# Optimization experiments

Measured on AMD Instinct MI355X. Metric: run time of the kernel, lower is better.

The kernel has to match this reference:

```python
import jax, jax.numpy as jnp
import numpy as np

EMBED_DIM = 1024
NUM_HEADS = 16
HEAD_DIM = EMBED_DIM // NUM_HEADS
SCALE = float(np.sqrt(HEAD_DIM))


def setup_inputs() -> dict:
    key = jax.random.key(0)
    ks = jax.random.split(key, 7)
    B, S, E = 2, 2048, EMBED_DIM
    query = jax.random.normal(ks[0], (B, S, E), dtype=jnp.float32)
    key_t = jax.random.normal(ks[1], (B, S, E), dtype=jnp.float32)
    value = jax.random.normal(ks[2], (B, S, E), dtype=jnp.float32)
    # nn.Linear(E, E, bias=False): weight shape (out, in); y = x @ W.T
    std = 1.0 / np.sqrt(E)
    Wq = jax.random.uniform(ks[3], (E, E), jnp.float32, -std, std)
    Wk = jax.random.uniform(ks[4], (E, E), jnp.float32, -std, std)
    Wv = jax.random.uniform(ks[5], (E, E), jnp.float32, -std, std)
    Wo = jax.random.uniform(ks[6], (E, E), jnp.float32, -std, std)
    return {"query": query, "key": key_t, "value": value,
            "Wq": Wq, "Wk": Wk, "Wv": Wv, "Wo": Wo}


def reference(query, key, value, Wq, Wk, Wv, Wo):
    B, S, E = query.shape
    H, D = NUM_HEADS, HEAD_DIM
    q = (query @ Wq.T).reshape(B, S, H, D).transpose(0, 2, 1, 3)  # [B,H,S,D]
    k = (key @ Wk.T).reshape(B, S, H, D).transpose(0, 2, 1, 3)
    v = (value @ Wv.T).reshape(B, S, H, D).transpose(0, 2, 1, 3)
    scores = jnp.einsum('bhqd,bhkd->bhqk', q, k) / SCALE  # [B,H,S,S]
    attn = jax.nn.softmax(scores, axis=-1)
    out = jnp.einsum('bhqk,bhkd->bhqd', attn, v)  # [B,H,S,D]
    out = out.transpose(0, 2, 1, 3).reshape(B, S, E)
    return out @ Wo.T
```

## Files before the change

### kernel.cpp

```cpp
#include <hip/hip_runtime.h>
#include <hip/hip_bf16.h>
#include <math.h>

typedef float f32x4 __attribute__((ext_vector_type(4)));
typedef __bf16 bf16x8 __attribute__((ext_vector_type(8)));
typedef unsigned short u16;
typedef u16 u16x8 __attribute__((ext_vector_type(8)));
typedef u16 u16x4 __attribute__((ext_vector_type(4)));

__device__ __forceinline__ u16 f2bf(float f) {
    unsigned u = __builtin_bit_cast(unsigned, f);
    u = (u + 0x7fffu + ((u >> 16) & 1u)) >> 16;
    return (u16)u;
}
__device__ __forceinline__ unsigned pack2_rhu(float a, float b) {
    return __builtin_amdgcn_perm(__builtin_bit_cast(unsigned, b) + 0x8000u,
                                 __builtin_bit_cast(unsigned, a) + 0x8000u,
                                 0x07060302u);
}

#if __has_builtin(__builtin_amdgcn_exp2f)
#define EXP2(x) __builtin_amdgcn_exp2f(x)
#else
#define EXP2(x) exp2f(x)
#endif

__device__ __forceinline__ void gload16(const u16* g, u16* l) {
    __builtin_amdgcn_global_load_lds(
        (const __attribute__((address_space(1))) unsigned int*)(g),
        (__attribute__((address_space(3))) unsigned int*)(l), 16, 0, 0);
}

__global__ __launch_bounds__(256) void cast_all(
    const float* __restrict__ q, const float* __restrict__ k, const float* __restrict__ v,
    const float* __restrict__ wq, const float* __restrict__ wk, const float* __restrict__ wv,
    const float* __restrict__ wo, u16* __restrict__ dst) {
    int i = blockIdx.x * 256 + threadIdx.x;
    const float* src;
    int off;
    if (i < 3145728) {
        int seg = i >> 20;
        src = (seg == 0) ? q : (seg == 1) ? k : v;
        off = i - (seg << 20);
    } else {
        int j = (i - 3145728) >> 18;
        src = (j == 0) ? wq : (j == 1) ? wk : (j == 2) ? wv : wo;
        off = (i - 3145728) - (j << 18);
    }
    float4 val = ((const float4*)src)[off];
    u16x4 o4;
    o4.x = f2bf(val.x); o4.y = f2bf(val.y); o4.z = f2bf(val.z); o4.w = f2bf(val.w);
    ((u16x4*)dst)[i] = o4;
}

__global__ __launch_bounds__(256) void qkv_gemm(
    const u16* __restrict__ Xq, const u16* __restrict__ Xk, const u16* __restrict__ Xv,
    const u16* __restrict__ Wq, const u16* __restrict__ Wk, const u16* __restrict__ Wv,
    u16* __restrict__ Qo, u16* __restrict__ Ko, u16* __restrict__ Vto) {
    constexpr int K = 1024;
    constexpr int BUF = 128 * 64;
    const int blk = blockIdx.x;
    const int xb = blk / 96;
    const int zb = (blk % 96) >> 5;
    const int yb = blk & 31;
    const int z = zb;
    const u16* __restrict__ A = (z == 0) ? Xq : (z == 1) ? Xk : Xv;
    const u16* __restrict__ W = (z == 0) ? Wq : (z == 1) ? Wk : Wv;
    u16* __restrict__ Out = (z == 0) ? Qo : (z == 1) ? Ko : Vto;

    __shared__ __align__(16) u16 As[2 * BUF];
    __shared__ __align__(16) u16 Bs[2 * BUF];

    const int t = threadIdx.x;
    const int lane = t & 63, wave = t >> 6;
    const int quad = lane >> 4, c = lane & 15, cx = c & 7;
    const int wr = (wave >> 1) * 64, wc = (wave & 1) * 64;
    const int rowA0 = yb * 128;
    const int colB0 = xb * 128;

    const int l3 = lane >> 3, l7 = lane & 7;
    const int chs = (l7 ^ l3) << 3;
    const u16* gA[4];
    const u16* gB[4];
    u16* lA[4];
    u16* lB[4];
#pragma unroll
    for (int i = 0; i < 4; ++i) {
        int row = wave * 32 + i * 8 + l3;
        gA[i] = A + (size_t)(rowA0 + row) * K + chs;
        gB[i] = W + (size_t)(colB0 + row) * K + chs;
        lA[i] = As + (wave * 256 + i * 64) * 8;
        lB[i] = Bs + (wave * 256 + i * 64) * 8;
    }

    const f32x4 zero4 = {0.f, 0.f, 0.f, 0.f};
    f32x4 acc[4][4];
#pragma unroll
    for (int i = 0; i < 4; ++i)
#pragma unroll
        for (int j = 0; j < 4; ++j) acc[i][j] = zero4;

#pragma unroll
    for (int i = 0; i < 4; ++i) {
        gload16(gA[i], lA[i]);
        gload16(gB[i], lB[i]);
    }

    for (int it = 0; it < 16; ++it) {
        __syncthreads();
        if (it + 1 < 16) {
            const int nb = ((it + 1) & 1) * BUF;
            const int kt = (it + 1) * 64;
#pragma unroll
            for (int i = 0; i < 4; ++i) {
                gload16(gA[i] + kt, lA[i] + nb);
                gload16(gB[i] + kt, lB[i] + nb);
            }
        }
        const int so = (it & 1) * BUF;
#pragma unroll
        for (int ks = 0; ks < 2; ++ks) {
            const int co = ((ks * 4 + quad) ^ cx) << 3;
            bf16x8 af[4], bfr[4];
#pragma unroll
            for (int i = 0; i < 4; ++i)
                af[i] = *(const bf16x8*)(As + so + (wr + i * 16 + c) * 64 + co);
#pragma unroll
            for (int j = 0; j < 4; ++j)
                bfr[j] = *(const bf16x8*)(Bs + so + (wc + j * 16 + c) * 64 + co);
            if (z == 2) {
#pragma unroll
                for (int i = 0; i < 4; ++i)
#pragma unroll
                    for (int j = 0; j < 4; ++j)
                        acc[i][j] = __builtin_amdgcn_mfma_f32_16x16x32_bf16(bfr[j], af[i], acc[i][j], 0, 0, 0);
            } else {
#pragma unroll
                for (int i = 0; i < 4; ++i)
#pragma unroll
                    for (int j = 0; j < 4; ++j)
                        acc[i][j] = __builtin_amdgcn_mfma_f32_16x16x32_bf16(af[i], bfr[j], acc[i][j], 0, 0, 0);
            }
        }
    }

    const float scale = (z == 0) ? 0.18033688011112042f : 1.0f;
#pragma unroll
    for (int i = 0; i < 4; ++i) {
#pragma unroll
        for (int j = 0; j < 4; ++j) {
#pragma unroll
            for (int r = 0; r < 4; ++r) {
                float v = acc[i][j][r];
                if (z == 2) {
                    int n = colB0 + wc + j * 16 + quad * 4 + r;
                    int m = rowA0 + wr + i * 16 + c;
                    int b = m >> 11, s = m & 2047, h = n >> 6, d = n & 63;
                    Out[((((b << 4) | h) << 6) + d) * 2048 + s] = f2bf(v);
                } else {
                    int m = rowA0 + wr + i * 16 + quad * 4 + r;
                    int n = colB0 + wc + j * 16 + c;
                    int b = m >> 11, s = m & 2047, h = n >> 6, d = n & 63;
                    Out[((((b << 4) | h) * 2048 + s) << 6) + d] = f2bf(v * scale);
                }
            }
        }
    }
}

__global__ __launch_bounds__(256) void out_gemm(const u16* __restrict__ A,
                                                const u16* __restrict__ W,
                                                float* __restrict__ Out) {
    constexpr int K = 1024;
    constexpr int ABUF = 64 * 64;
    constexpr int BBUF = 128 * 64;
    __shared__ __align__(16) u16 As[2 * ABUF];
    __shared__ __align__(16) u16 Bs[2 * BBUF];
    const int blk = blockIdx.x;
    const int yb = blk & 63;
    const int xb = blk >> 6;
    const int t = threadIdx.x;
    const int lane = t & 63, wave = t >> 6;
    const int quad = lane >> 4, c = lane & 15, cx = c & 7;
    const int wr = (wave >> 1) * 32, wc = (wave & 1) * 64;
    const int rowA0 = yb * 64;
    const int colB0 = xb * 128;

    const int l3 = lane >> 3, l7 = lane & 7;
    const int chs = (l7 ^ l3) << 3;
    const u16* gA[2];
    const u16* gB[4];
    u16* lA[2];
    u16* lB[4];
#pragma unroll
    for (int i = 0; i < 2; ++i) {
        int row = wave * 16 + i * 8 + l3;
        gA[i] = A + (size_t)(rowA0 + row) * K + chs;
        lA[i] = As + (wave * 128 + i * 64) * 8;
    }
#pragma unroll
    for (int i = 0; i < 4; ++i) {
        int row = wave * 32 + i * 8 + l3;
        gB[i] = W + (size_t)(colB0 + row) * K + chs;
        lB[i] = Bs + (wave * 256 + i * 64) * 8;
    }

    const f32x4 zero4 = {0.f, 0.f, 0.f, 0.f};
    f32x4 acc[2][4];
#pragma unroll
    for (int i = 0; i < 2; ++i)
#pragma unroll
        for (int j = 0; j < 4; ++j) acc[i][j] = zero4;

#pragma unroll
    for (int i = 0; i < 2; ++i) gload16(gA[i], lA[i]);
#pragma unroll
    for (int i = 0; i < 4; ++i) gload16(gB[i], lB[i]);

    for (int it = 0; it < 16; ++it) {
        __syncthreads();
        if (it + 1 < 16) {
            const int kt = (it + 1) * 64;
            const int nsel = (it + 1) & 1;
#pragma unroll
            for (int i = 0; i < 2; ++i) gload16(gA[i] + kt, lA[i] + nsel * ABUF);
#pragma unroll
            for (int i = 0; i < 4; ++i) gload16(gB[i] + kt, lB[i] + nsel * BBUF);
        }
        const int soA = (it & 1) * ABUF;
        const int soB = (it & 1) * BBUF;
#pragma unroll
        for (int ks = 0; ks < 2; ++ks) {
            const int co = ((ks * 4 + quad) ^ cx) << 3;
            bf16x8 af[2], bfr[4];
#pragma unroll
            for (int i = 0; i < 2; ++i)
                af[i] = *(const bf16x8*)(As + soA + (wr + i * 16 + c) * 64 + co);
#pragma unroll
            for (int j = 0; j < 4; ++j)
                bfr[j] = *(const bf16x8*)(Bs + soB + (wc + j * 16 + c) * 64 + co);
#pragma unroll
            for (int i = 0; i < 2; ++i)
#pragma unroll
                for (int j = 0; j < 4; ++j)
                    acc[i][j] = __builtin_amdgcn_mfma_f32_16x16x32_bf16(af[i], bfr[j], acc[i][j], 0, 0, 0);
        }
    }
#pragma unroll
    for (int i = 0; i < 2; ++i)
#pragma unroll
        for (int j = 0; j < 4; ++j)
#pragma unroll
            for (int r = 0; r < 4; ++r) {
                int m = rowA0 + wr + i * 16 + quad * 4 + r;
                int n = colB0 + wc + j * 16 + c;
                Out[(m << 10) + n] = acc[i][j][r];
            }
}

__global__ __launch_bounds__(512) void flash_attn(const u16* __restrict__ Qp,
                                                  const u16* __restrict__ Kp,
                                                  const u16* __restrict__ Vt,
                                                  u16* __restrict__ Ob) {
    constexpr int S = 2048;
    const int blk = blockIdx.x;
    const int bh = ((blk & 7) << 2) | ((blk >> 3) & 3);
    const int b = bh >> 4, h = bh & 15;
    const int t = threadIdx.x, wave = t >> 6, lane = t & 63;
    const int quad = lane >> 4, c = lane & 15, cx = c & 7;
    const int qw = (blk >> 5) * 256 + wave * 32;
    const u16* Qb = Qp + (bh * S + qw) * 64;
    const u16* Kb = Kp + (bh * S) * 64;
    const u16* Vb = Vt + bh * 64 * S;

    __shared__ __align__(16) u16 Ks[2][64 * 64];
    __shared__ __align__(16) u16 Vs[2][64 * 64];
    __shared__ __align__(16) u16 Ps[8][32 * 64];
    u16* Pw = &Ps[wave][0];

    bf16x8 qf[2][2];
#pragma unroll
    for (int qt = 0; qt < 2; ++qt)
#pragma unroll
        for (int hf = 0; hf < 2; ++hf)
            qf[qt][hf] = *(const bf16x8*)(Qb + (qt * 16 + c) * 64 + hf * 32 + quad * 8);

    u16x8 ou;
#pragma unroll
    for (int i = 0; i < 8; ++i) ou[i] = 0x3F80;
    const bf16x8 onesf = __builtin_bit_cast(bf16x8, ou);

    const int l3 = lane >> 3, l7 = lane & 7;
    const int chs = (l7 ^ l3) << 3;
    const int row = wave * 8 + l3;
    const u16* gK = Kb + row * 64 + chs;
    const u16* gV = Vb + row * 2048 + chs;
    const int lbase = wave * 512;

    gload16(gK, &Ks[0][lbase]);
    gload16(gV, &Vs[0][lbase]);
    __syncthreads();

    const f32x4 zero4 = {0.f, 0.f, 0.f, 0.f};
    f32x4 o[2][4];
    f32x4 ol[2];
#pragma unroll
    for (int qt = 0; qt < 2; ++qt) {
        ol[qt] = zero4;
#pragma unroll
        for (int t2 = 0; t2 < 4; ++t2) o[qt][t2] = zero4;
    }

    const int co0 = (quad ^ cx) << 3, co1 = ((4 + quad) ^ cx) << 3;

    for (int it = 0; it < S / 64; ++it) {
        const int cur = it & 1;
        if (it + 1 < S / 64) {
            gload16(gK + (it + 1) * 4096, &Ks[cur ^ 1][lbase]);
            gload16(gV + (it + 1) * 64, &Vs[cur ^ 1][lbase]);
        }
        const u16* Kc = &Ks[cur][0];
        const u16* Vc = &Vs[cur][0];
        f32x4 sc[4][2];
#pragma unroll
        for (int kt = 0; kt < 4; ++kt) {
            const int krow = (kt * 16 + c) * 64;
            bf16x8 kf0 = *(const bf16x8*)(Kc + krow + co0);
            bf16x8 kf1 = *(const bf16x8*)(Kc + krow + co1);
#pragma unroll
            for (int qt = 0; qt < 2; ++qt) {
                f32x4 zz = zero4;
                zz = __builtin_amdgcn_mfma_f32_16x16x32_bf16(kf0, qf[qt][0], zz, 0, 0, 0);
                zz = __builtin_amdgcn_mfma_f32_16x16x32_bf16(kf1, qf[qt][1], zz, 0, 0, 0);
                sc[kt][qt] = zz;
            }
        }
#pragma unroll
        for (int kt = 0; kt < 4; ++kt) {
            const int pchunk = ((kt * 2 + (quad >> 1)) ^ cx) << 3;
#pragma unroll
            for (int qt = 0; qt < 2; ++qt) {
                float p0 = EXP2(sc[kt][qt][0]);
                float p1 = EXP2(sc[kt][qt][1]);
                float p2 = EXP2(sc[kt][qt][2]);
                float p3 = EXP2(sc[kt][qt][3]);
                uint2 pk;
                pk.x = pack2_rhu(p0, p1);
                pk.y = pack2_rhu(p2, p3);
                *(uint2*)(Pw + (qt * 16 + c) * 64 + pchunk + (quad & 1) * 4) = pk;
            }
        }
        __asm__ __volatile__("s_waitcnt lgkmcnt(0)" ::: "memory");
        bf16x8 pf[2][2];
#pragma unroll
        for (int qt = 0; qt < 2; ++qt) {
            pf[qt][0] = *(const bf16x8*)(Pw + (qt * 16 + c) * 64 + co0);
            pf[qt][1] = *(const bf16x8*)(Pw + (qt * 16 + c) * 64 + co1);
        }
#pragma unroll
        for (int qt = 0; qt < 2; ++qt) {
            ol[qt] = __builtin_amdgcn_mfma_f32_16x16x32_bf16(pf[qt][0], onesf, ol[qt], 0, 0, 0);
            ol[qt] = __builtin_amdgcn_mfma_f32_16x16x32_bf16(pf[qt][1], onesf, ol[qt], 0, 0, 0);
        }
#pragma unroll
        for (int t2 = 0; t2 < 4; ++t2) {
            const int vrow = (t2 * 16 + c) * 64;
            bf16x8 vf0 = *(const bf16x8*)(Vc + vrow + co0);
            bf16x8 vf1 = *(const bf16x8*)(Vc + vrow + co1);
#pragma unroll
            for (int qt = 0; qt < 2; ++qt) {
                o[qt][t2] = __builtin_amdgcn_mfma_f32_16x16x32_bf16(pf[qt][0], vf0, o[qt][t2], 0, 0, 0);
                o[qt][t2] = __builtin_amdgcn_mfma_f32_16x16x32_bf16(pf[qt][1], vf1, o[qt][t2], 0, 0, 0);
            }
        }
        __syncthreads();
    }
#pragma unroll
    for (int qt = 0; qt < 2; ++qt)
#pragma unroll
        for (int r = 0; r < 4; ++r) {
            float inv = 1.f / ol[qt][r];
            int rw = qw + qt * 16 + quad * 4 + r;
            int base = ((b * S + rw) * 16 + h) * 64;
#pragma unroll
            for (int t2 = 0; t2 < 4; ++t2)
                Ob[base + t2 * 16 + c] = f2bf(o[qt][t2][r] * inv);
        }
}

extern "C" void kernel_launch(void* const* d_in, const int* in_sizes, int n_in,
                              void* d_out, int out_size, void* d_ws, size_t ws_size,
                              hipStream_t stream) {
    const float* q  = (const float*)d_in[0];
    const float* k  = (const float*)d_in[1];
    const float* v  = (const float*)d_in[2];
    const float* wq = (const float*)d_in[3];
    const float* wk = (const float*)d_in[4];
    const float* wv = (const float*)d_in[5];
    const float* wo = (const float*)d_in[6];

    u16* ws = (u16*)d_ws;
    u16* qb  = ws;
    u16* kb  = ws + 4194304;
    u16* vb  = ws + 8388608;
    u16* wqb = ws + 12582912;
    u16* wkb = ws + 13631488;
    u16* wvb = ws + 14680064;
    u16* wob = ws + 15728640;
    u16* Qp  = ws + 16777216;
    u16* Kp  = ws + 20971520;
    u16* Vtp = ws + 25165824;
    u16* Obf = ws + 29360128;

    cast_all<<<16384, 256, 0, stream>>>(q, k, v, wq, wk, wv, wo, ws);

    qkv_gemm<<<768, 256, 0, stream>>>(qb, kb, vb, wqb, wkb, wvb, Qp, Kp, Vtp);

    flash_attn<<<256, 512, 0, stream>>>(Qp, Kp, Vtp, Obf);

    out_gemm<<<512, 256, 0, stream>>>(Obf, wob, (float*)d_out);
}
```

Baseline: 216.5 us.

## Keep P in registers using 16x16x16 MFMA and halve attention block size

The attention kernel no longer writes the exp'd score tile P to LDS and reads it back. The score MFMA output layout is reused directly as the A operand of 16x16x16 bf16 MFMAs, and V fragments are read with matching swizzled 4-element loads. Blocks shrink from 8 waves to 4 with twice as many blocks, and each thread issues two K/V async loads per tile. This removes the P LDS round trip and its waitcnt, but doubles the MFMA instruction count at half the K depth and adds more, smaller LDS reads for V.

```diff
diff --git a/kernel.cpp b/kernel.cpp
--- a/kernel.cpp
+++ b/kernel.cpp
@@ -4,6 +4,8 @@
 
 typedef float f32x4 __attribute__((ext_vector_type(4)));
 typedef __bf16 bf16x8 __attribute__((ext_vector_type(8)));
+typedef __bf16 bf16x4 __attribute__((ext_vector_type(4)));
+typedef short s16x4 __attribute__((ext_vector_type(4)));
 typedef unsigned short u16;
 typedef u16 u16x8 __attribute__((ext_vector_type(8)));
 typedef u16 u16x4 __attribute__((ext_vector_type(4)));
@@ -24,6 +26,15 @@
 #else
 #define EXP2(x) exp2f(x)
 #endif
+
+__device__ __forceinline__ f32x4 mfma16(bf16x4 a, bf16x4 b, f32x4 c) {
+#if __has_builtin(__builtin_amdgcn_mfma_f32_16x16x16_bf16)
+    return __builtin_amdgcn_mfma_f32_16x16x16_bf16(a, b, c, 0, 0, 0);
+#else
+    return __builtin_amdgcn_mfma_f32_16x16x16bf16_1k(
+        __builtin_bit_cast(s16x4, a), __builtin_bit_cast(s16x4, b), c, 0, 0, 0);
+#endif
+}
 
 __device__ __forceinline__ void gload16(const u16* g, u16* l) {
     __builtin_amdgcn_global_load_lds(
@@ -258,25 +269,24 @@
             }
 }
 
-__global__ __launch_bounds__(512) void flash_attn(const u16* __restrict__ Qp,
+__global__ __launch_bounds__(256) void flash_attn(const u16* __restrict__ Qp,
                                                   const u16* __restrict__ Kp,
                                                   const u16* __restrict__ Vt,
                                                   u16* __restrict__ Ob) {
     constexpr int S = 2048;
     const int blk = blockIdx.x;
-    const int bh = ((blk & 7) << 2) | ((blk >> 3) & 3);
+    const int j = blk & 31;
+    const int bh = ((j & 7) << 2) | (j >> 3);
     const int b = bh >> 4, h = bh & 15;
     const int t = threadIdx.x, wave = t >> 6, lane = t & 63;
     const int quad = lane >> 4, c = lane & 15, cx = c & 7;
-    const int qw = (blk >> 5) * 256 + wave * 32;
+    const int qw = (blk >> 5) * 128 + wave * 32;
     const u16* Qb = Qp + (bh * S + qw) * 64;
     const u16* Kb = Kp + (bh * S) * 64;
     const u16* Vb = Vt + bh * 64 * S;
 
     __shared__ __align__(16) u16 Ks[2][64 * 64];
     __shared__ __align__(16) u16 Vs[2][64 * 64];
-    __shared__ __align__(16) u16 Ps[8][32 * 64];
-    u16* Pw = &Ps[wave][0];
 
     bf16x8 qf[2][2];
 #pragma unroll
@@ -285,20 +295,28 @@
         for (int hf = 0; hf < 2; ++hf)
             qf[qt][hf] = *(const bf16x8*)(Qb + (qt * 16 + c) * 64 + hf * 32 + quad * 8);
 
-    u16x8 ou;
-#pragma unroll
-    for (int i = 0; i < 8; ++i) ou[i] = 0x3F80;
-    const bf16x8 onesf = __builtin_bit_cast(bf16x8, ou);
+    u16x4 ou;
+#pragma unroll
+    for (int i = 0; i < 4; ++i) ou[i] = 0x3F80;
+    const bf16x4 ones4 = __builtin_bit_cast(bf16x4, ou);
 
     const int l3 = lane >> 3, l7 = lane & 7;
     const int chs = (l7 ^ l3) << 3;
-    const int row = wave * 8 + l3;
-    const u16* gK = Kb + row * 64 + chs;
-    const u16* gV = Vb + row * 2048 + chs;
-    const int lbase = wave * 512;
-
-    gload16(gK, &Ks[0][lbase]);
-    gload16(gV, &Vs[0][lbase]);
+    const u16* gK[2];
+    const u16* gV[2];
+    int lbase[2];
+#pragma unroll
+    for (int i = 0; i < 2; ++i) {
+        int row = wave * 16 + i * 8 + l3;
+        gK[i] = Kb + row * 64 + chs;
+        gV[i] = Vb + row * 2048 + chs;
+        lbase[i] = (wave * 128 + i * 64) * 8;
+    }
+#pragma unroll
+    for (int i = 0; i < 2; ++i) {
+        gload16(gK[i], &Ks[0][lbase[i]]);
+        gload16(gV[i], &Vs[0][lbase[i]]);
+    }
     __syncthreads();
 
     const f32x4 zero4 = {0.f, 0.f, 0.f, 0.f};
@@ -316,8 +334,11 @@
     for (int it = 0; it < S / 64; ++it) {
         const int cur = it & 1;
         if (it + 1 < S / 64) {
-            gload16(gK + (it + 1) * 4096, &Ks[cur ^ 1][lbase]);
-            gload16(gV + (it + 1) * 64, &Vs[cur ^ 1][lbase]);
+#pragma unroll
+            for (int i = 0; i < 2; ++i) {
+                gload16(gK[i] + (it + 1) * 4096, &Ks[cur ^ 1][lbase[i]]);
+                gload16(gV[i] + (it + 1) * 64, &Vs[cur ^ 1][lbase[i]]);
+            }
         }
         const u16* Kc = &Ks[cur][0];
         const u16* Vc = &Vs[cur][0];
@@ -335,9 +356,9 @@
                 sc[kt][qt] = zz;
             }
         }
-#pragma unroll
-        for (int kt = 0; kt < 4; ++kt) {
-            const int pchunk = ((kt * 2 + (quad >> 1)) ^ cx) << 3;
+        bf16x4 pa[4][2];
+#pragma unroll
+        for (int kt = 0; kt < 4; ++kt)
 #pragma unroll
             for (int qt = 0; qt < 2; ++qt) {
                 float p0 = EXP2(sc[kt][qt][0]);
@@ -347,30 +368,23 @@
                 uint2 pk;
                 pk.x = pack2_rhu(p0, p1);
                 pk.y = pack2_rhu(p2, p3);
-                *(uint2*)(Pw + (qt * 16 + c) * 64 + pchunk + (quad & 1) * 4) = pk;
-            }
-        }
-        __asm__ __volatile__("s_waitcnt lgkmcnt(0)" ::: "memory");
-        bf16x8 pf[2][2];
-#pragma unroll
-        for (int qt = 0; qt < 2; ++qt) {
-            pf[qt][0] = *(const bf16x8*)(Pw + (qt * 16 + c) * 64 + co0);
-            pf[qt][1] = *(const bf16x8*)(Pw + (qt * 16 + c) * 64 + co1);
-        }
-#pragma unroll
-        for (int qt = 0; qt < 2; ++qt) {
-            ol[qt] = __builtin_amdgcn_mfma_f32_16x16x32_bf16(pf[qt][0], onesf, ol[qt], 0, 0, 0);
-            ol[qt] = __builtin_amdgcn_mfma_f32_16x16x32_bf16(pf[qt][1], onesf, ol[qt], 0, 0, 0);
-        }
+                pa[kt][qt] = __builtin_bit_cast(bf16x4, pk);
+            }
+#pragma unroll
+        for (int kt = 0; kt < 4; ++kt)
+#pragma unroll
+            for (int qt = 0; qt < 2; ++qt)
+                ol[qt] = mfma16(pa[kt][qt], ones4, ol[qt]);
 #pragma unroll
         for (int t2 = 0; t2 < 4; ++t2) {
             const int vrow = (t2 * 16 + c) * 64;
-            bf16x8 vf0 = *(const bf16x8*)(Vc + vrow + co0);
-            bf16x8 vf1 = *(const bf16x8*)(Vc + vrow + co1);
-#pragma unroll
-            for (int qt = 0; qt < 2; ++qt) {
-                o[qt][t2] = __builtin_amdgcn_mfma_f32_16x16x32_bf16(pf[qt][0], vf0, o[qt][t2], 0, 0, 0);
-                o[qt][t2] = __builtin_amdgcn_mfma_f32_16x16x32_bf16(pf[qt][1], vf1, o[qt][t2], 0, 0, 0);
+#pragma unroll
+            for (int kt = 0; kt < 4; ++kt) {
+                const int vphys = ((kt * 2 + (quad >> 1)) ^ cx) << 3;
+                bf16x4 vf = *(const bf16x4*)(Vc + vrow + vphys + (quad & 1) * 4);
+#pragma unroll
+                for (int qt = 0; qt < 2; ++qt)
+                    o[qt][t2] = mfma16(pa[kt][qt], vf, o[qt][t2]);
             }
         }
         __syncthreads();
@@ -380,8 +394,8 @@
 #pragma unroll
         for (int r = 0; r < 4; ++r) {
             float inv = 1.f / ol[qt][r];
-            int rw = qw + qt * 16 + quad * 4 + r;
-            int base = ((b * S + rw) * 16 + h) * 64;
+            int row = qw + qt * 16 + quad * 4 + r;
+            int base = ((b * S + row) * 16 + h) * 64;
 #pragma unroll
             for (int t2 = 0; t2 < 4; ++t2)
                 Ob[base + t2 * 16 + c] = f2bf(o[qt][t2][r] * inv);
@@ -416,7 +430,7 @@
 
     qkv_gemm<<<768, 256, 0, stream>>>(qb, kb, vb, wqb, wkb, wvb, Qp, Kp, Vtp);
 
-    flash_attn<<<256, 512, 0, stream>>>(Qp, Kp, Vtp, Obf);
+    flash_attn<<<512, 256, 0, stream>>>(Qp, Kp, Vtp, Obf);
 
     out_gemm<<<512, 256, 0, stream>>>(Obf, wob, (float*)d_out);
 }
```

New measurement: 224.8 us. 1.04x slower.
